# Kernel tuning notes

Hardware: AMD Instinct MI355X
Metric: run time of the kernel (lower is better)

## Reference

```python
import jax, jax.numpy as jnp
import numpy as np

N, E, F, P, G, H, T = 50000, 800000, 512, 128, 256, 256, 24


def setup_inputs() -> dict:
    key = jax.random.key(0)
    ks = jax.random.split(key, 16)
    sc = lambda k, shape, fan: jax.random.normal(k, shape, jnp.float32) / np.sqrt(fan)
    return {
        "x": jax.random.normal(ks[0], (N, F), jnp.float32),
        "edge_index": jax.random.randint(ks[1], (2, E), 0, N),
        "feat_gate": jax.random.uniform(ks[2], (F,), jnp.float32),
        "edge_gate": jax.random.uniform(ks[3], (E,), jnp.float32),
        "cached_gcn": jax.random.normal(ks[4], (T, 2 * G), jnp.float32),
        "W_proj": sc(ks[5], (F, P), F), "b_proj": jnp.zeros((P,), jnp.float32),
        "W_g1": sc(ks[6], (P, G), P), "b_g1": jnp.zeros((G,), jnp.float32),
        "W_g2": sc(ks[7], (G, G), G), "b_g2": jnp.zeros((G,), jnp.float32),
        "W_ih": sc(ks[8], (2 * G, 4 * H), 2 * G), "W_hh": sc(ks[9], (H, 4 * H), H),
        "b_ih": jnp.zeros((4 * H,), jnp.float32), "b_hh": jnp.zeros((4 * H,), jnp.float32),
        "W_att": sc(ks[10], (H, 1), H), "b_att": jnp.zeros((1,), jnp.float32),
        "W_p1": sc(ks[11], (H, 64), H), "b_p1": jnp.zeros((64,), jnp.float32),
        "W_p2": sc(ks[12], (64, 1), 64), "b_p2": jnp.zeros((1,), jnp.float32),
        "target_idx": 12345,
        "explain_pos": 5,
    }


def gcn_conv(h, src, dst, w, W, b, n_nodes):
    # PyG GCNConv: linear, add self-loops (weight 1), sym norm, aggregate, bias
    h = h @ W
    deg = jnp.zeros((n_nodes,), h.dtype).at[dst].add(w) + 1.0  # self-loop adds 1
    dinv = jax.lax.rsqrt(deg)
    norm = dinv[src] * w * dinv[dst]
    out = jax.ops.segment_sum(norm[:, None] * h[src], dst, num_segments=n_nodes)
    out = out + h * (dinv * dinv)[:, None]  # self-loop message
    return out + b


def lstm(seq, W_ih, W_hh, b_ih, b_hh):
    hd = W_hh.shape[0]
    def step(carry, xt):
        h, c = carry
        g = xt @ W_ih + h @ W_hh + b_ih + b_hh
        i, f, gg, o = jnp.split(g, 4)
        i, f, o = jax.nn.sigmoid(i), jax.nn.sigmoid(f), jax.nn.sigmoid(o)
        c = f * c + i * jnp.tanh(gg)
        h = o * jnp.tanh(c)
        return (h, c), h
    init = (jnp.zeros((hd,), seq.dtype), jnp.zeros((hd,), seq.dtype))
    _, outs = jax.lax.scan(step, init, seq)
    return outs  # [T, H]


def reference(x, edge_index, feat_gate, edge_gate, cached_gcn,
              W_proj, b_proj, W_g1, b_g1, W_g2, b_g2,
              W_ih, W_hh, b_ih, b_hh, W_att, b_att,
              W_p1, b_p1, W_p2, b_p2, target_idx, explain_pos):
    src, dst = edge_index[0], edge_index[1]
    n_nodes = x.shape[0]
    # feat_mask_scope='all': gate every node's features
    xm = x * feat_gate[None, :]
    p = jax.nn.relu(xm @ W_proj + b_proj)
    # edge_mask_scope='all': edge weights are the gate itself
    h1 = jax.nn.relu(gcn_conv(p, src, dst, edge_gate, W_g1, b_g1, n_nodes))
    h2 = jax.nn.relu(gcn_conv(h1, src, dst, edge_gate, W_g2, b_g2, n_nodes))
    tgt_emb = jnp.concatenate([h1[target_idx], h2[target_idx]])  # [2G]
    seq = cached_gcn.at[explain_pos].set(tgt_emb)                 # [T, 2G]
    rnn_out = lstm(seq, W_ih, W_hh, b_ih, b_hh)                   # [T, H]
    scores = jnp.tanh(rnn_out @ W_att + b_att)                    # [T, 1]
    attw = jax.nn.softmax(scores, axis=0)
    ctx = jnp.sum(rnn_out * attw, axis=0)                         # [H]
    hid = jax.nn.relu(ctx @ W_p1 + b_p1)                          # dropout inactive (eval)
    raw = (hid @ W_p2 + b_p2)[0]
    return jax.nn.softplus(raw)
```

## Files before the change

kernel.cpp:

```cpp
#include <hip/hip_runtime.h>
#include <math.h>

constexpr int N = 50000, E = 800000, F = 512, P = 128, G = 256, H = 256, T = 24;
constexpr int CAPA = 4096, CAPB = 32768, CAPP = 2048, CAPH = 512;

constexpr size_t OFF_DEG   = 0;
constexpr size_t OFF_CNT   = 200704;
constexpr size_t OFF_COMM  = 200768;
constexpr size_t OFF_FH1   = 204864;
constexpr size_t OFF_FP    = 254912;
constexpr size_t ZERO_END  = 304960;
constexpr size_t OFF_IDXP  = 304960;
constexpr size_t OFF_IDXH1 = 504960;
constexpr size_t OFF_SRCA  = 704960;
constexpr size_t OFF_WA    = 721344;
constexpr size_t OFF_SRCB  = 737728;
constexpr size_t OFF_DSTB  = 868800;
constexpr size_t OFF_WB    = 999872;
constexpr size_t OFF_LISTP = 1130944;
constexpr size_t OFF_LISTH = 1139136;
constexpr size_t OFF_Q     = 1141184;
constexpr size_t OFF_RS    = 3238336;
constexpr size_t OFF_EMB   = 3762624;
constexpr size_t OFF_XPROJ = 3764672;

__device__ __forceinline__ float fsig_(float x) {
    return __builtin_amdgcn_rcpf(1.0f + __expf(-x));
}
__device__ __forceinline__ float ftanh_(float x) {
    return 1.0f - 2.0f * __builtin_amdgcn_rcpf(1.0f + __expf(2.0f * x));
}

__global__ void k_scan1(const int* __restrict__ ei, const float* __restrict__ eg,
                        const int* __restrict__ ptgt, int* __restrict__ cnt,
                        unsigned char* __restrict__ fH1,
                        int* __restrict__ srcA, float* __restrict__ wA) {
    int target = *ptgt;
    int base = (blockIdx.x * 256 + threadIdx.x) * 4;
    if (base < E) {
        int4 d4 = *(const int4*)&ei[E + base];
        int dd0 = d4.x, dd1 = d4.y, dd2 = d4.z, dd3 = d4.w;
        #pragma unroll
        for (int j = 0; j < 4; j++) {
            int d = (j == 0) ? dd0 : (j == 1) ? dd1 : (j == 2) ? dd2 : dd3;
            if (d == target) {
                int e = base + j;
                int s = ei[e];
                int slot = atomicAdd(&cnt[0], 1);
                if (slot < CAPA) { srcA[slot] = s; wA[slot] = eg[e]; }
                fH1[s] = 1;
            }
        }
    }
    if (blockIdx.x == 0 && threadIdx.x == 0) fH1[target] = 1;
}

__global__ void k_scan2(const int* __restrict__ ei, const float* __restrict__ eg,
                        const unsigned char* __restrict__ fH1, unsigned char* __restrict__ fP,
                        int* __restrict__ cnt, int* __restrict__ srcB,
                        int* __restrict__ dstB, float* __restrict__ wB,
                        float* __restrict__ deg) {
    int base = (blockIdx.x * 256 + threadIdx.x) * 4;
    if (base >= E) return;
    int4 d4 = *(const int4*)&ei[E + base];
    int dd0 = d4.x, dd1 = d4.y, dd2 = d4.z, dd3 = d4.w;
    #pragma unroll
    for (int j = 0; j < 4; j++) {
        int d = (j == 0) ? dd0 : (j == 1) ? dd1 : (j == 2) ? dd2 : dd3;
        if (fH1[d]) {
            int e = base + j;
            int s = ei[e];
            float w = eg[e];
            int slot = atomicAdd(&cnt[1], 1);
            if (slot < CAPB) { srcB[slot] = s; dstB[slot] = d; wB[slot] = w; }
            fP[s] = 1;
            atomicAdd(&deg[d], w);
        }
    }
}

__global__ void k_scan3c(const int* __restrict__ ei, const float* __restrict__ eg,
                         const unsigned char* __restrict__ fH1, const unsigned char* __restrict__ fP,
                         float* __restrict__ deg, int* __restrict__ cnt,
                         int* __restrict__ listP, int* __restrict__ listH,
                         int* __restrict__ idxP, int* __restrict__ idxH1) {
    int base = (blockIdx.x * 256 + threadIdx.x) * 4;
    if (base < E) {
        int4 d4 = *(const int4*)&ei[E + base];
        int dd0 = d4.x, dd1 = d4.y, dd2 = d4.z, dd3 = d4.w;
        #pragma unroll
        for (int j = 0; j < 4; j++) {
            int d = (j == 0) ? dd0 : (j == 1) ? dd1 : (j == 2) ? dd2 : dd3;
            if (fP[d] && !fH1[d]) atomicAdd(&deg[d], eg[base + j]);
        }
    }
    int n = blockIdx.x * 256 + threadIdx.x;
    if (n < N) {
        if (fH1[n]) {
            int sh = atomicAdd(&cnt[3], 1);
            if (sh < CAPH) listH[sh] = n;
            idxH1[n] = sh;
        }
        if (fP[n] || fH1[n]) {
            int sp = atomicAdd(&cnt[2], 1);
            if (sp < CAPP) listP[sp] = n;
            idxP[n] = sp;
        }
    }
}

__global__ void k_pq(const float* __restrict__ x, const float* __restrict__ fgate,
                     const float* __restrict__ Wproj, const float* __restrict__ bproj,
                     const float* __restrict__ Wg1, const int* __restrict__ cnt,
                     const int* __restrict__ listP, float* __restrict__ q) {
    __shared__ float xm[F];
    __shared__ float part[256];
    __shared__ float pv[P];
    int nP = min(cnt[2], CAPP);
    int tid = threadIdx.x;
    for (int row = blockIdx.x; row < nP; row += 256) {
        int n = listP[row];
        __syncthreads();
        for (int i = tid; i < F; i += 256) xm[i] = x[(size_t)n * F + i] * fgate[i];
        __syncthreads();
        int col = tid & 127, kh = tid >> 7;
        const float* wp = Wproj + (size_t)(kh * 256) * P + col;
        const float* xh = xm + kh * 256;
        float acc = 0.0f;
        #pragma unroll 16
        for (int k = 0; k < 256; k++) acc += xh[k] * wp[(size_t)k * P];
        part[tid] = acc;
        __syncthreads();
        if (tid < P) pv[tid] = fmaxf(part[tid] + part[tid + 128] + bproj[tid], 0.0f);
        __syncthreads();
        float a = 0.0f;
        #pragma unroll 16
        for (int k = 0; k < P; k++) a += pv[k] * Wg1[k * G + tid];
        q[(size_t)row * G + tid] = a;
    }
}

__global__ void k_h1(const int* __restrict__ ptgt, const float* __restrict__ deg,
                     const int* __restrict__ cnt, const int* __restrict__ listH,
                     const int* __restrict__ idxP, const int* __restrict__ srcB,
                     const int* __restrict__ dstB, const float* __restrict__ wB,
                     const float* __restrict__ q, const float* __restrict__ bg1,
                     const float* __restrict__ Wg2,
                     float* __restrict__ rs, float* __restrict__ emb) {
    __shared__ float h1row[G];
    __shared__ int ldst[512];
    __shared__ int lsrc[512];
    __shared__ float lw[512];
    int b = blockIdx.x;
    int nH = min(cnt[3], CAPH);
    if (b >= nH) return;
    int n = listH[b];
    int target = *ptgt;
    int g = threadIdx.x;
    float dn = rsqrtf(deg[n] + 1.0f);
    float acc = bg1[g] + q[(size_t)idxP[n] * G + g] * dn * dn;
    int nB = min(cnt[1], CAPB);
    for (int base = 0; base < nB; base += 512) {
        int m = min(512, nB - base);
        __syncthreads();
        for (int i = g; i < m; i += 256) {
            int s2 = srcB[base + i];
            ldst[i] = dstB[base + i];
            lsrc[i] = s2;
            lw[i] = wB[base + i] * rsqrtf(deg[s2] + 1.0f);
        }
        __syncthreads();
        for (int e = 0; e < m; e++) {
            if (ldst[e] == n)
                acc += lw[e] * dn * q[(size_t)idxP[lsrc[e]] * G + g];
        }
    }
    float hv = fmaxf(acc, 0.0f);
    h1row[g] = hv;
    if (n == target) emb[g] = hv;
    __syncthreads();
    float r = 0.0f;
    #pragma unroll 8
    for (int k = 0; k < G; k++) r += h1row[k] * Wg2[k * G + g];
    rs[(size_t)b * G + g] = r;
}

__global__ void k_xproj(const float* __restrict__ cached, const float* __restrict__ emb,
                        const int* __restrict__ ptgt, const int* __restrict__ pepos,
                        const float* __restrict__ deg, const int* __restrict__ cnt,
                        const int* __restrict__ idxH1, const int* __restrict__ srcA,
                        const float* __restrict__ wA, const float* __restrict__ rs,
                        const float* __restrict__ bg2,
                        const float* __restrict__ Wih, const float* __restrict__ bih,
                        const float* __restrict__ bhh, float* __restrict__ xproj) {
    __shared__ float s[T][2 * G];
    int tid = threadIdx.x;
    int epos = *pepos;
    for (int i = tid; i < T * 2 * G; i += 256) {
        int t = i >> 9, k = i & 511;
        s[t][k] = (t == epos && k < G) ? emb[k] : cached[i];
    }
    int target = *ptgt;
    float dt = rsqrtf(deg[target] + 1.0f);
    float h2v = 0.0f;
    if (tid < G) {
        int it = idxH1[target];
        h2v = bg2[tid] + rs[(size_t)it * G + tid] * dt * dt;
        int nA = min(cnt[0], CAPA);
        for (int e = 0; e < nA; e++) {
            int sn = srcA[e];
            h2v += rsqrtf(deg[sn] + 1.0f) * wA[e] * dt * rs[(size_t)idxH1[sn] * G + tid];
        }
    }
    __syncthreads();
    if (tid < G) s[epos][G + tid] = fmaxf(h2v, 0.0f);
    __syncthreads();
    int col = blockIdx.x * 32 + (tid & 31);
    int tg = tid >> 5;
    float base = bih[col] + bhh[col];
    float acc[3];
    #pragma unroll
    for (int i = 0; i < 3; i++) acc[i] = base;
    #pragma unroll 16
    for (int k = 0; k < 2 * G; k++) {
        float wv = Wih[k * 4 * H + col];
        #pragma unroll
        for (int i = 0; i < 3; i++) acc[i] += s[tg + i * 8][k] * wv;
    }
    #pragma unroll
    for (int i = 0; i < 3; i++) xproj[(tg + i * 8) * 4 * H + col] = acc[i];
}

typedef float fv16 __attribute__((ext_vector_type(16)));

#define LDE(J,Eidx) wv##J[Eidx] = Whh[(size_t)((J) * 16 + (Eidx)) * 1024 + col];
#define LDV(J) LDE(J,0) LDE(J,1) LDE(J,2) LDE(J,3) LDE(J,4) LDE(J,5) LDE(J,6) LDE(J,7) \
               LDE(J,8) LDE(J,9) LDE(J,10) LDE(J,11) LDE(J,12) LDE(J,13) LDE(J,14) LDE(J,15)

#define DOT4(J,Q,ACC) { float4 h4 = hb4[(J) * 4 + (Q)]; \
    ACC += h4.x * wv##J[4*(Q)] + h4.y * wv##J[4*(Q)+1] \
         + h4.z * wv##J[4*(Q)+2] + h4.w * wv##J[4*(Q)+3]; }
#define DOTV(J) DOT4(J,0,a0) DOT4(J,1,a1) DOT4(J,2,a2) DOT4(J,3,a3)

__global__ __launch_bounds__(256, 1) void k_lstm(
        const float* __restrict__ Whh, const float* __restrict__ xproj,
        unsigned long long* __restrict__ comm, int* __restrict__ ctrl,
        const float* __restrict__ Watt, const float* __restrict__ batt,
        const float* __restrict__ Wp1, const float* __restrict__ bp1,
        const float* __restrict__ Wp2, const float* __restrict__ bp2,
        float* __restrict__ out) {
    __shared__ __align__(16) float hbuf[H];
    __shared__ float glds[4 * 64];
    __shared__ float rnn_lds[T][H];
    __shared__ float sc[T];
    __shared__ float attw[T];
    __shared__ float ctx_l[H];
    __shared__ float watt_l[H];
    __shared__ float part[256];
    __shared__ float hid_l[64];
    __shared__ float wp2_l[64];
    __shared__ int role_s;

    int tid = threadIdx.x;

    if (tid == 0) {
        int xcd;
        asm volatile("s_getreg_b32 %0, hwreg(HW_REG_XCC_ID)" : "=s"(xcd));
        xcd &= 7;
        int role = -1;
        int ticket = __hip_atomic_fetch_add(&ctrl[xcd], 1, __ATOMIC_RELAXED,
                                            __HIP_MEMORY_SCOPE_AGENT);
        if (ticket < 4) {
            if (ticket == 3) {
                int expected = 0;
                __hip_atomic_compare_exchange_strong(&ctrl[8], &expected, xcd + 1,
                        __ATOMIC_RELAXED, __ATOMIC_RELAXED, __HIP_MEMORY_SCOPE_AGENT);
            }
            int wnr;
            do {
                wnr = __hip_atomic_load(&ctrl[8], __ATOMIC_RELAXED, __HIP_MEMORY_SCOPE_AGENT);
                __builtin_amdgcn_s_sleep(1);
            } while (wnr == 0);
            if (wnr == xcd + 1) role = ticket;
        }
        role_s = role;
    }
    __syncthreads();
    int w = role_s;
    if (w < 0) return;
    int l = tid & 63;
    int col = (tid >> 6) * H + w * 64 + l;

    fv16 wv0, wv1, wv2, wv3, wv4, wv5, wv6, wv7;
    fv16 wv8, wv9, wv10, wv11, wv12, wv13, wv14, wv15;
    LDV(0) LDV(1) LDV(2) LDV(3) LDV(4) LDV(5) LDV(6) LDV(7)
    LDV(8) LDV(9) LDV(10) LDV(11) LDV(12) LDV(13) LDV(14) LDV(15)

    int pch = tid + (tid >= w * 64 ? 64 : 0);

    const float4* hb4 = (const float4*)hbuf;
    hbuf[tid] = 0.0f;
    float cstate = 0.0f;
    float xnext = xproj[col];
    __syncthreads();

    for (int t = 0; t < T; t++) {
        float xt = xnext;
        if (t + 1 < T) xnext = xproj[(t + 1) * 4 * H + col];
        float a0 = 0.0f, a1 = 0.0f, a2 = 0.0f, a3 = 0.0f;
        DOTV(0) DOTV(1) DOTV(2) DOTV(3) DOTV(4) DOTV(5) DOTV(6) DOTV(7)
        DOTV(8) DOTV(9) DOTV(10) DOTV(11) DOTV(12) DOTV(13) DOTV(14) DOTV(15)
        glds[tid] = ((a0 + a1) + (a2 + a3)) + xt;
        __syncthreads();
        int s = t + 1;
        if (tid < 64) {
            float gi = glds[l], gf = glds[64 + l], gg = glds[128 + l], go = glds[192 + l];
            cstate = fsig_(gf) * cstate + fsig_(gi) * ftanh_(gg);
            float hv = fsig_(go) * ftanh_(cstate);
            unsigned long long word =
                ((unsigned long long)__float_as_uint(hv) << 32) | (unsigned)s;
            __hip_atomic_store(&comm[(size_t)(s & 1) * 256 + w * 64 + l], word,
                               __ATOMIC_RELAXED, __HIP_MEMORY_SCOPE_AGENT);
            hbuf[w * 64 + l] = hv;
        }
        if (tid < 192) {
            const unsigned long long* cp = &comm[(size_t)(s & 1) * 256 + pch];
            unsigned long long wd =
                __hip_atomic_load(cp, __ATOMIC_RELAXED, __HIP_MEMORY_SCOPE_AGENT);
            while ((unsigned)wd != (unsigned)s) {
                __builtin_amdgcn_s_sleep(1);
                wd = __hip_atomic_load(cp, __ATOMIC_RELAXED, __HIP_MEMORY_SCOPE_AGENT);
            }
            hbuf[pch] = __uint_as_float((unsigned)(wd >> 32));
        }
        __syncthreads();
        if (w == 0) rnn_lds[t][tid] = hbuf[tid];
    }

    if (w != 0) return;
    watt_l[tid] = Watt[tid];
    if (tid < 64) wp2_l[tid] = Wp2[tid];
    __syncthreads();
    if (tid < T) {
        float sv = 0.0f;
        #pragma unroll 8
        for (int h = 0; h < H; h++) sv += rnn_lds[tid][h] * watt_l[h];
        sc[tid] = tanhf(sv + batt[0]);
    }
    __syncthreads();
    if (tid == 0) {
        float m = -1e30f;
        for (int t = 0; t < T; t++) m = fmaxf(m, sc[t]);
        float su = 0.0f;
        for (int t = 0; t < T; t++) { float e = expf(sc[t] - m); attw[t] = e; su += e; }
        float inv = 1.0f / su;
        for (int t = 0; t < T; t++) attw[t] *= inv;
    }
    __syncthreads();
    {
        float a = 0.0f;
        #pragma unroll
        for (int t = 0; t < T; t++) a += rnn_lds[t][tid] * attw[t];
        ctx_l[tid] = a;
    }
    __syncthreads();
    {
        int col2 = tid & 63, sl2 = tid >> 6;
        float a = 0.0f;
        #pragma unroll 16
        for (int kk = 0; kk < 64; kk++) {
            int k = sl2 * 64 + kk;
            a += ctx_l[k] * Wp1[k * 64 + col2];
        }
        part[tid] = a;
    }
    __syncthreads();
    if (tid < 64) {
        float a = bp1[tid] + part[tid] + part[64 + tid] + part[128 + tid] + part[192 + tid];
        hid_l[tid] = fmaxf(a, 0.0f);
    }
    __syncthreads();
    if (tid == 0) {
        float r = bp2[0];
        #pragma unroll
        for (int j = 0; j < 64; j++) r += hid_l[j] * wp2_l[j];
        out[0] = (r > 20.0f) ? r : log1pf(expf(r));
    }
}

extern "C" void kernel_launch(void* const* d_in, const int* in_sizes, int n_in,
                              void* d_out, int out_size, void* d_ws, size_t ws_size,
                              hipStream_t stream) {
    const float* x      = (const float*)d_in[0];
    const int*   ei     = (const int*)d_in[1];
    const float* fgate  = (const float*)d_in[2];
    const float* egate  = (const float*)d_in[3];
    const float* cached = (const float*)d_in[4];
    const float* Wproj  = (const float*)d_in[5];
    const float* bproj  = (const float*)d_in[6];
    const float* Wg1    = (const float*)d_in[7];
    const float* bg1    = (const float*)d_in[8];
    const float* Wg2    = (const float*)d_in[9];
    const float* bg2    = (const float*)d_in[10];
    const float* Wih    = (const float*)d_in[11];
    const float* Whh    = (const float*)d_in[12];
    const float* bih    = (const float*)d_in[13];
    const float* bhh    = (const float*)d_in[14];
    const float* Watt   = (const float*)d_in[15];
    const float* batt   = (const float*)d_in[16];
    const float* Wp1    = (const float*)d_in[17];
    const float* bp1    = (const float*)d_in[18];
    const float* Wp2    = (const float*)d_in[19];
    const float* bp2    = (const float*)d_in[20];
    const int*   ptgt   = (const int*)d_in[21];
    const int*   pepos  = (const int*)d_in[22];

    char* ws = (char*)d_ws;
    float* deg   = (float*)(ws + OFF_DEG);
    int*   cnt   = (int*)(ws + OFF_CNT);
    unsigned long long* comm = (unsigned long long*)(ws + OFF_COMM);
    unsigned char* fH1 = (unsigned char*)(ws + OFF_FH1);
    unsigned char* fP  = (unsigned char*)(ws + OFF_FP);
    int*   idxP  = (int*)(ws + OFF_IDXP);
    int*   idxH1 = (int*)(ws + OFF_IDXH1);
    int*   srcA  = (int*)(ws + OFF_SRCA);
    float* wA    = (float*)(ws + OFF_WA);
    int*   srcB  = (int*)(ws + OFF_SRCB);
    int*   dstB  = (int*)(ws + OFF_DSTB);
    float* wB    = (float*)(ws + OFF_WB);
    int*   listP = (int*)(ws + OFF_LISTP);
    int*   listH = (int*)(ws + OFF_LISTH);
    float* q     = (float*)(ws + OFF_Q);
    float* rs    = (float*)(ws + OFF_RS);
    float* emb   = (float*)(ws + OFF_EMB);
    float* xproj = (float*)(ws + OFF_XPROJ);

    hipMemsetAsync(ws, 0, ZERO_END, stream);

    int nEB = (E / 4 + 255) / 256;
    k_scan1<<<nEB, 256, 0, stream>>>(ei, egate, ptgt, cnt, fH1, srcA, wA);
    k_scan2<<<nEB, 256, 0, stream>>>(ei, egate, fH1, fP, cnt, srcB, dstB, wB, deg);
    k_scan3c<<<nEB, 256, 0, stream>>>(ei, egate, fH1, fP, deg, cnt, listP, listH, idxP, idxH1);
    k_pq<<<256, 256, 0, stream>>>(x, fgate, Wproj, bproj, Wg1, cnt, listP, q);
    k_h1<<<CAPH, 256, 0, stream>>>(ptgt, deg, cnt, listH, idxP, srcB, dstB, wB, q, bg1, Wg2, rs, emb);
    k_xproj<<<32, 256, 0, stream>>>(cached, emb, ptgt, pepos, deg, cnt, idxH1, srcA, wA, rs, bg2,
                                    Wih, bih, bhh, xproj);
    k_lstm<<<64, 256, 0, stream>>>(Whh, xproj, comm, cnt + 4, Watt, batt, Wp1, bp1, Wp2, bp2,
                                   (float*)d_out);
}
```

Before: 153.7 us.

## Precompute cached-row input projections alongside pq, leave only target row late

The 23 non-target timesteps of the LSTM input projection do not depend on the GCN results, so their Wih products are now computed by 32 extra blocks attached to the pq kernel. The later kernel then only computes the h2 aggregation and a single-row projection for the explain position, using a split-K reduction across warps. This takes the large T×2G×4H GEMV off the serial critical path after k_h1. The cost is larger shared memory in the merged kernel, which may lower occupancy for the pq blocks.

```diff
diff --git a/kernel.cpp b/kernel.cpp
--- a/kernel.cpp
+++ b/kernel.cpp
@@ -109,34 +109,58 @@
     }
 }
 
-__global__ void k_pq(const float* __restrict__ x, const float* __restrict__ fgate,
-                     const float* __restrict__ Wproj, const float* __restrict__ bproj,
-                     const float* __restrict__ Wg1, const int* __restrict__ cnt,
-                     const int* __restrict__ listP, float* __restrict__ q) {
-    __shared__ float xm[F];
-    __shared__ float part[256];
-    __shared__ float pv[P];
-    int nP = min(cnt[2], CAPP);
+__global__ void k_pq_x(const float* __restrict__ x, const float* __restrict__ fgate,
+                       const float* __restrict__ Wproj, const float* __restrict__ bproj,
+                       const float* __restrict__ Wg1, const int* __restrict__ cnt,
+                       const int* __restrict__ listP, float* __restrict__ q,
+                       const float* __restrict__ cached, const int* __restrict__ pepos,
+                       const float* __restrict__ Wih, const float* __restrict__ bih,
+                       const float* __restrict__ bhh, float* __restrict__ xproj) {
+    __shared__ __align__(16) char smem[49152];
     int tid = threadIdx.x;
-    for (int row = blockIdx.x; row < nP; row += 256) {
-        int n = listP[row];
+    int bid = blockIdx.x;
+    if (bid < 256) {
+        float* xm   = (float*)smem;
+        float* part = xm + F;
+        float* pv   = part + 256;
+        int nP = min(cnt[2], CAPP);
+        for (int row = bid; row < nP; row += 256) {
+            int n = listP[row];
+            __syncthreads();
+            for (int i = tid; i < F; i += 256) xm[i] = x[(size_t)n * F + i] * fgate[i];
+            __syncthreads();
+            int col = tid & 127, kh = tid >> 7;
+            const float* wp = Wproj + (size_t)(kh * 256) * P + col;
+            const float* xh = xm + kh * 256;
+            float acc = 0.0f;
+            #pragma unroll 16
+            for (int k = 0; k < 256; k++) acc += xh[k] * wp[(size_t)k * P];
+            part[tid] = acc;
+            __syncthreads();
+            if (tid < P) pv[tid] = fmaxf(part[tid] + part[tid + 128] + bproj[tid], 0.0f);
+            __syncthreads();
+            float a = 0.0f;
+            #pragma unroll 16
+            for (int k = 0; k < P; k++) a += pv[k] * Wg1[k * G + tid];
+            q[(size_t)row * G + tid] = a;
+        }
+    } else {
+        float (*s)[2 * G] = (float(*)[2 * G])smem;
+        int epos = *pepos;
+        for (int i = tid; i < T * 2 * G; i += 256) s[i >> 9][i & 511] = cached[i];
         __syncthreads();
-        for (int i = tid; i < F; i += 256) xm[i] = x[(size_t)n * F + i] * fgate[i];
-        __syncthreads();
-        int col = tid & 127, kh = tid >> 7;
-        const float* wp = Wproj + (size_t)(kh * 256) * P + col;
-        const float* xh = xm + kh * 256;
-        float acc = 0.0f;
+        int col = (bid - 256) * 32 + (tid & 31);
+        int tg = tid >> 5;
+        float base = bih[col] + bhh[col];
+        float a0 = base, a1 = base, a2 = base;
         #pragma unroll 16
-        for (int k = 0; k < 256; k++) acc += xh[k] * wp[(size_t)k * P];
-        part[tid] = acc;
-        __syncthreads();
-        if (tid < P) pv[tid] = fmaxf(part[tid] + part[tid + 128] + bproj[tid], 0.0f);
-        __syncthreads();
-        float a = 0.0f;
-        #pragma unroll 16
-        for (int k = 0; k < P; k++) a += pv[k] * Wg1[k * G + tid];
-        q[(size_t)row * G + tid] = a;
+        for (int k = 0; k < 2 * G; k++) {
+            float wv = Wih[k * 4 * H + col];
+            a0 += s[tg][k] * wv; a1 += s[tg + 8][k] * wv; a2 += s[tg + 16][k] * wv;
+        }
+        if (tg != epos)      xproj[tg * 4 * H + col] = a0;
+        if (tg + 8 != epos)  xproj[(tg + 8) * 4 * H + col] = a1;
+        if (tg + 16 != epos) xproj[(tg + 16) * 4 * H + col] = a2;
     }
 }
 
@@ -185,50 +209,47 @@
     rs[(size_t)b * G + g] = r;
 }
 
-__global__ void k_xproj(const float* __restrict__ cached, const float* __restrict__ emb,
-                        const int* __restrict__ ptgt, const int* __restrict__ pepos,
-                        const float* __restrict__ deg, const int* __restrict__ cnt,
-                        const int* __restrict__ idxH1, const int* __restrict__ srcA,
-                        const float* __restrict__ wA, const float* __restrict__ rs,
-                        const float* __restrict__ bg2,
+__global__ void k_xpost(const float* __restrict__ emb, const int* __restrict__ ptgt,
+                        const int* __restrict__ pepos, const float* __restrict__ deg,
+                        const int* __restrict__ cnt, const int* __restrict__ idxH1,
+                        const int* __restrict__ srcA, const float* __restrict__ wA,
+                        const float* __restrict__ rs, const float* __restrict__ bg2,
                         const float* __restrict__ Wih, const float* __restrict__ bih,
                         const float* __restrict__ bhh, float* __restrict__ xproj) {
-    __shared__ float s[T][2 * G];
+    __shared__ float se[2 * G];
+    __shared__ float red[256];
     int tid = threadIdx.x;
-    int epos = *pepos;
-    for (int i = tid; i < T * 2 * G; i += 256) {
-        int t = i >> 9, k = i & 511;
-        s[t][k] = (t == epos && k < G) ? emb[k] : cached[i];
-    }
-    int target = *ptgt;
+    int target = *ptgt, epos = *pepos;
     float dt = rsqrtf(deg[target] + 1.0f);
-    float h2v = 0.0f;
     if (tid < G) {
+        se[tid] = emb[tid];
         int it = idxH1[target];
-        h2v = bg2[tid] + rs[(size_t)it * G + tid] * dt * dt;
+        float h2v = bg2[tid] + rs[(size_t)it * G + tid] * dt * dt;
         int nA = min(cnt[0], CAPA);
         for (int e = 0; e < nA; e++) {
             int sn = srcA[e];
             h2v += rsqrtf(deg[sn] + 1.0f) * wA[e] * dt * rs[(size_t)idxH1[sn] * G + tid];
         }
-    }
-    __syncthreads();
-    if (tid < G) s[epos][G + tid] = fmaxf(h2v, 0.0f);
+        se[G + tid] = fmaxf(h2v, 0.0f);
+    }
     __syncthreads();
     int col = blockIdx.x * 32 + (tid & 31);
-    int tg = tid >> 5;
-    float base = bih[col] + bhh[col];
-    float acc[3];
-    #pragma unroll
-    for (int i = 0; i < 3; i++) acc[i] = base;
+    int ks = tid >> 5;
+    float a = 0.0f;
     #pragma unroll 16
-    for (int k = 0; k < 2 * G; k++) {
-        float wv = Wih[k * 4 * H + col];
+    for (int kk = 0; kk < 64; kk++) {
+        int k = ks * 64 + kk;
+        a += se[k] * Wih[k * 4 * H + col];
+    }
+    red[tid] = a;
+    __syncthreads();
+    if (tid < 32) {
+        int c2 = blockIdx.x * 32 + tid;
+        float s2 = bih[c2] + bhh[c2];
         #pragma unroll
-        for (int i = 0; i < 3; i++) acc[i] += s[tg + i * 8][k] * wv;
-    }
-    #pragma unroll
-    for (int i = 0; i < 3; i++) xproj[(tg + i * 8) * 4 * H + col] = acc[i];
+        for (int j = 0; j < 8; j++) s2 += red[j * 32 + tid];
+        xproj[epos * 4 * H + c2] = s2;
+    }
 }
 
 typedef float fv16 __attribute__((ext_vector_type(16)));
@@ -441,9 +462,10 @@
     k_scan1<<<nEB, 256, 0, stream>>>(ei, egate, ptgt, cnt, fH1, srcA, wA);
     k_scan2<<<nEB, 256, 0, stream>>>(ei, egate, fH1, fP, cnt, srcB, dstB, wB, deg);
     k_scan3c<<<nEB, 256, 0, stream>>>(ei, egate, fH1, fP, deg, cnt, listP, listH, idxP, idxH1);
-    k_pq<<<256, 256, 0, stream>>>(x, fgate, Wproj, bproj, Wg1, cnt, listP, q);
+    k_pq_x<<<288, 256, 0, stream>>>(x, fgate, Wproj, bproj, Wg1, cnt, listP, q,
+                                    cached, pepos, Wih, bih, bhh, xproj);
     k_h1<<<CAPH, 256, 0, stream>>>(ptgt, deg, cnt, listH, idxP, srcB, dstB, wB, q, bg1, Wg2, rs, emb);
-    k_xproj<<<32, 256, 0, stream>>>(cached, emb, ptgt, pepos, deg, cnt, idxH1, srcA, wA, rs, bg2,
+    k_xpost<<<32, 256, 0, stream>>>(emb, ptgt, pepos, deg, cnt, idxH1, srcA, wA, rs, bg2,
                                     Wih, bih, bhh, xproj);
     k_lstm<<<64, 256, 0, stream>>>(Whh, xproj, comm, cnt + 4, Watt, batt, Wp1, bp1, Wp2, bp2,
                                    (float*)d_out);
```

New measurement: 150.5 us. -2.1%, faster.
